# Performance work log

Measured on AMD Instinct MI355X. Metric: run time of the kernel, lower is better.

Reference implementation:

```python
import jax, jax.numpy as jnp
import numpy as np

B, C, H, W = 32, 3, 512, 512


def _make_rot(N):
    k = np.arange(N, dtype=np.float64)[None, :] * np.pi / (2 * N)
    return jnp.asarray(np.cos(k), jnp.float32), jnp.asarray(np.sin(k), jnp.float32)


def setup_inputs() -> dict:
    key = jax.random.key(0)
    X = jax.random.normal(key, (B, C, H, W), dtype=jnp.float32)
    W_r_weight, W_i_weight = _make_rot(W)
    W_r_height, W_i_height = _make_rot(H)
    return {
        "X": X,
        "W_r_weight": W_r_weight,
        "W_i_weight": W_i_weight,
        "W_r_height": W_r_height,
        "W_i_height": W_i_height,
    }


def _idct1(X, W_r, W_i):
    # 1D IDCT (DCT-III) along last axis via irfft, norm='ortho'.
    shp = X.shape
    N = shp[-1]
    Xv = X.reshape(-1, N) * 0.5
    # ortho scaling: col 0 -> *sqrt(N)*2, cols 1: -> *sqrt(N/2)*2 (after the /2)
    col_scale = np.full((N,), np.sqrt(N / 2) * 2, dtype=np.float32)
    col_scale[0] = np.sqrt(N) * 2
    Xv = Xv * jnp.asarray(col_scale)
    # V_t_i[:, 0] = 0; V_t_i[:, j] = -Xv[:, N-j] for j >= 1
    Vti = jnp.concatenate([jnp.zeros_like(Xv[:, :1]), -Xv[:, :0:-1]], axis=1)
    Vr = Xv * W_r - Vti * W_i
    Vi = Xv * W_i + Vti * W_r
    v = jnp.fft.irfft(jax.lax.complex(Vr, Vi), n=N, axis=1)  # [M, N] real
    # de-interleave: even outputs from front half, odd outputs from reversed tail
    x = jnp.zeros_like(v)
    x = x.at[:, ::2].set(v[:, : N - N // 2])
    x = x.at[:, 1::2].set(v[:, ::-1][:, : N // 2])
    return x.reshape(shp)


def reference(X, W_r_weight, W_i_weight, W_r_height, W_i_height):
    x = _idct1(X, W_r_weight, W_i_weight)          # IDCT over width
    x = jnp.swapaxes(x, -1, -2)
    x = _idct1(x, W_r_height, W_i_height)          # IDCT over height
    return jnp.swapaxes(x, -1, -2)
```

## Files before the change

### kernel.cpp

```cpp
#include <hip/hip_runtime.h>
#include <math.h>
#include <stdint.h>

#define N512 512

typedef __attribute__((ext_vector_type(8))) short short8;
typedef __attribute__((ext_vector_type(4))) float floatx4;

#define VMCNT0 asm volatile("s_waitcnt vmcnt(0)" ::: "memory")

__device__ __forceinline__ short f2bf(float f) {
    uint32_t u = __float_as_uint(f);
    uint32_t r = u + 0x7fffu + ((u >> 16) & 1u);
    return (short)(r >> 16);
}

__device__ __forceinline__ short f2bf_fast(float f) {
    return (short)((__float_as_uint(f) + 0x8000u) >> 16);
}

__device__ __forceinline__ void gload_lds16(const void* g, void* l) {
    __builtin_amdgcn_global_load_lds(
        (const __attribute__((address_space(1))) void*)g,
        (__attribute__((address_space(3))) void*)l,
        16, 0, 0);
}

__device__ __forceinline__ void decode_wave(int id, int& ms, int& ps, int& z) {
    const int g = (id >> 6) * 8 + (id & 7);
    ms = (id >> 3) & 7;
    ps = g & 7;
    z  = g >> 3;
}

__global__ __launch_bounds__(256) void build_idct_matrix_bf16(short* __restrict__ M) {
    int idx = blockIdx.x * 256 + threadIdx.x;
    int n = idx >> 9;
    int k = idx & 511;
    int j = (k * (2 * n + 1)) & (4 * N512 - 1);
    float theta = (float)j * (3.14159265358979323846f / (2.0f * (float)N512));
    float s = (k == 0) ? 0.044194173824159216f : 0.0625f;
    M[idx] = f2bf(s * cosf(theta));
}

__global__ __launch_bounds__(64) void gemm_s1(const short* __restrict__ A,
                                              const float* __restrict__ Xg,
                                              short* __restrict__ Tg) {
    __shared__ __align__(16) short ldsA[8 * 512];
    __shared__ __align__(16) short ldsB[8 * 512];

    const int l = threadIdx.x;
    const int q = (l >> 4) & 3;
    const int r = l & 15;

    int ms, ps, z;
    decode_wave(blockIdx.x, ms, ps, z);
    const int m0 = ms * 64;
    const int n0 = ps * 64;

    const float* Xs = Xg + ((long)z << 18);
    short* Tt = Tg + ((long)z << 18);

    const int rsub = l >> 3;
    const int glog = (l & 7) ^ rsub;

    const int brow = l >> 4;

    floatx4 acc[4][4] = {};
    float4 v[16];

    for (int kt = 0; kt < 8; ++kt) {
        const int k0 = kt * 64;
#pragma unroll
        for (int i = 0; i < 8; ++i)
            gload_lds16(A + (((long)(m0 + i * 8 + rsub)) << 9) + k0 + glog * 8,
                        ldsA + i * 512);
#pragma unroll
        for (int e = 0; e < 16; ++e) {
            const int rt = e * 4 + brow;
            v[e] = *(const float4*)(Xs + (((long)(n0 + rt)) << 9) + k0 + r * 4);
        }
        VMCNT0;
#pragma unroll
        for (int e = 0; e < 16; ++e) {
            const int rt = e * 4 + brow;
            short4 o;
            o.x = f2bf_fast(v[e].x);
            o.y = f2bf_fast(v[e].y);
            o.z = f2bf_fast(v[e].z);
            o.w = f2bf_fast(v[e].w);
            *(short4*)(ldsB + rt * 64 + (((r >> 1) ^ (rt & 7)) * 8) + (r & 1) * 4) = o;
        }
#pragma unroll
        for (int kk = 0; kk < 2; ++kk) {
            const int c = kk * 4 + q;
            const int goff = ((c ^ (r & 7)) * 8);
            short8 af[4], bfr[4];
#pragma unroll
            for (int i = 0; i < 4; ++i) {
                af[i]  = *(const short8*)(ldsA + (i * 16 + r) * 64 + goff);
                bfr[i] = *(const short8*)(ldsB + (i * 16 + r) * 64 + goff);
            }
#pragma unroll
            for (int i = 0; i < 4; ++i)
#pragma unroll
                for (int j = 0; j < 4; ++j)
                    acc[i][j] = __builtin_amdgcn_mfma_f32_16x16x32_bf16(
                        af[i], bfr[j], acc[i][j], 0, 0, 0);
        }
    }

#pragma unroll
    for (int i = 0; i < 4; ++i) {
        const int mrow = m0 + i * 16 + q * 4;
#pragma unroll
        for (int j = 0; j < 4; ++j) {
            const int ncol = n0 + j * 16 + r;
#pragma unroll
            for (int rg = 0; rg < 4; ++rg)
                Tt[(long)(mrow + rg) * N512 + ncol] = f2bf(acc[i][j][rg]);
        }
    }
}

__global__ __launch_bounds__(64) void gemm_s2(const short* __restrict__ A,
                                              const short* __restrict__ Bg,
                                              float* __restrict__ Cg) {
    __shared__ __align__(16) short ldsA[8 * 512];
    __shared__ __align__(16) short ldsB[8 * 512];

    const int l = threadIdx.x;
    const int q = (l >> 4) & 3;
    const int r = l & 15;

    int ms, ps, z;
    decode_wave(blockIdx.x, ms, ps, z);
    const int m0 = ms * 64;
    const int n0 = ps * 64;

    const short* Bs = Bg + ((long)z << 18);
    float* C = Cg + ((long)z << 18);

    const int rsub = l >> 3;
    const int glog = (l & 7) ^ rsub;

    floatx4 acc[4][4] = {};

    for (int kt = 0; kt < 8; ++kt) {
        const int k0 = kt * 64;
#pragma unroll
        for (int i = 0; i < 8; ++i) {
            gload_lds16(A + (((long)(m0 + i * 8 + rsub)) << 9) + k0 + glog * 8,
                        ldsA + i * 512);
            gload_lds16(Bs + (((long)(n0 + i * 8 + rsub)) << 9) + k0 + glog * 8,
                        ldsB + i * 512);
        }
        VMCNT0;
#pragma unroll
        for (int kk = 0; kk < 2; ++kk) {
            const int c = kk * 4 + q;
            const int goff = ((c ^ (r & 7)) * 8);
            short8 af[4], bfr[4];
#pragma unroll
            for (int i = 0; i < 4; ++i) {
                af[i]  = *(const short8*)(ldsA + (i * 16 + r) * 64 + goff);
                bfr[i] = *(const short8*)(ldsB + (i * 16 + r) * 64 + goff);
            }
#pragma unroll
            for (int i = 0; i < 4; ++i)
#pragma unroll
                for (int j = 0; j < 4; ++j)
                    acc[i][j] = __builtin_amdgcn_mfma_f32_16x16x32_bf16(
                        af[i], bfr[j], acc[i][j], 0, 0, 0);
        }
    }

#pragma unroll
    for (int i = 0; i < 4; ++i) {
        const int mrow = m0 + i * 16 + q * 4;
#pragma unroll
        for (int j = 0; j < 4; ++j) {
            const int ncol = n0 + j * 16 + r;
#pragma unroll
            for (int rg = 0; rg < 4; ++rg)
                C[(long)(mrow + rg) * N512 + ncol] = acc[i][j][rg];
        }
    }
}

extern "C" void kernel_launch(void* const* d_in, const int* in_sizes, int n_in,
                              void* d_out, int out_size, void* d_ws, size_t ws_size,
                              hipStream_t stream) {
    const float* X = (const float*)d_in[0];
    float* out = (float*)d_out;

    const long plane = (long)N512 * N512;
    const int slices = in_sizes[0] / (int)plane;

    short* Mb = (short*)d_ws;
    short* Tt = Mb + plane;

    long avail = (long)ws_size - plane * 2;
    int chunk = (int)(avail / (plane * 2));
    if (chunk > slices) chunk = slices;
    if (chunk < 1) chunk = 1;

    build_idct_matrix_bf16<<<dim3((int)(plane / 256)), dim3(256), 0, stream>>>(Mb);

    for (int s0 = 0; s0 < slices; s0 += chunk) {
        int c = (s0 + chunk <= slices) ? chunk : (slices - s0);
        gemm_s1<<<dim3(64 * c), dim3(64), 0, stream>>>(
            Mb, X + (long)s0 * plane, Tt);
        gemm_s2<<<dim3(64 * c), dim3(64), 0, stream>>>(
            Mb, Tt, out + (long)s0 * plane);
    }
}
```

Measured before the change: 259.1 us.

## Use 256x256 block tiles with 8 waves and double-buffered LDS pipelining

```diff
diff --git a/kernel.cpp b/kernel.cpp
--- a/kernel.cpp
+++ b/kernel.cpp
@@ -7,7 +7,9 @@
 typedef __attribute__((ext_vector_type(8))) short short8;
 typedef __attribute__((ext_vector_type(4))) float floatx4;
 
-#define VMCNT0 asm volatile("s_waitcnt vmcnt(0)" ::: "memory")
+#define VMCNT0  asm volatile("s_waitcnt vmcnt(0)" ::: "memory")
+#define LGKM0   asm volatile("s_waitcnt lgkmcnt(0)" ::: "memory")
+#define BARRIER __builtin_amdgcn_s_barrier()
 
 __device__ __forceinline__ short f2bf(float f) {
     uint32_t u = __float_as_uint(f);
@@ -24,13 +26,6 @@
         (const __attribute__((address_space(1))) void*)g,
         (__attribute__((address_space(3))) void*)l,
         16, 0, 0);
-}
-
-__device__ __forceinline__ void decode_wave(int id, int& ms, int& ps, int& z) {
-    const int g = (id >> 6) * 8 + (id & 7);
-    ms = (id >> 3) & 7;
-    ps = g & 7;
-    z  = g >> 3;
 }
 
 __global__ __launch_bounds__(256) void build_idct_matrix_bf16(short* __restrict__ M) {
@@ -43,20 +38,45 @@
     M[idx] = f2bf(s * cosf(theta));
 }
 
-__global__ __launch_bounds__(64) void gemm_s1(const short* __restrict__ A,
-                                              const float* __restrict__ Xg,
-                                              short* __restrict__ Tg) {
-    __shared__ __align__(16) short ldsA[8 * 512];
-    __shared__ __align__(16) short ldsB[8 * 512];
-
-    const int l = threadIdx.x;
+#define QUAD(MF)                                                                \
+    do {                                                                        \
+        short8 a00 = *(const short8*)(bufcA + (wm0 + (MF)*16 + r)*64 + gq0);    \
+        short8 a01 = *(const short8*)(bufcA + (wm0 + (MF)*16 + r)*64 + gq1);    \
+        short8 a10 = *(const short8*)(bufcA + (wm0 + (MF)*16 + 16 + r)*64 + gq0);\
+        short8 a11 = *(const short8*)(bufcA + (wm0 + (MF)*16 + 16 + r)*64 + gq1);\
+        __builtin_amdgcn_s_setprio(1);                                          \
+        _Pragma("unroll")                                                       \
+        for (int nf = 0; nf < 4; ++nf) {                                        \
+            acc[(MF)][nf]     = __builtin_amdgcn_mfma_f32_16x16x32_bf16(        \
+                a00, bfr[nf][0], acc[(MF)][nf], 0, 0, 0);                       \
+            acc[(MF)][nf]     = __builtin_amdgcn_mfma_f32_16x16x32_bf16(        \
+                a01, bfr[nf][1], acc[(MF)][nf], 0, 0, 0);                       \
+            acc[(MF) + 1][nf] = __builtin_amdgcn_mfma_f32_16x16x32_bf16(        \
+                a10, bfr[nf][0], acc[(MF) + 1][nf], 0, 0, 0);                   \
+            acc[(MF) + 1][nf] = __builtin_amdgcn_mfma_f32_16x16x32_bf16(        \
+                a11, bfr[nf][1], acc[(MF) + 1][nf], 0, 0, 0);                   \
+        }                                                                       \
+        __builtin_amdgcn_s_setprio(0);                                          \
+    } while (0)
+
+__global__ __launch_bounds__(512, 2) void gemm_s1(const short* __restrict__ A,
+                                                  const float* __restrict__ Xg,
+                                                  short* __restrict__ Tg) {
+    __shared__ __align__(16) short lds[2 * 32768];
+
+    const int t = threadIdx.x;
+    const int wv = t >> 6;
+    const int l = t & 63;
     const int q = (l >> 4) & 3;
     const int r = l & 15;
 
-    int ms, ps, z;
-    decode_wave(blockIdx.x, ms, ps, z);
-    const int m0 = ms * 64;
-    const int n0 = ps * 64;
+    const int id = blockIdx.x;
+    const int bn0 = (id & 1) * 256;
+    const int bm0 = ((id >> 1) & 1) * 256;
+    const int z = id >> 2;
+
+    const int wm0 = (wv >> 2) * 128;
+    const int wn0 = (wv & 3) * 64;
 
     const float* Xs = Xg + ((long)z << 18);
     short* Tt = Tg + ((long)z << 18);
@@ -64,79 +84,123 @@
     const int rsub = l >> 3;
     const int glog = (l & 7) ^ rsub;
 
-    const int brow = l >> 4;
-
-    floatx4 acc[4][4] = {};
-    float4 v[16];
+    const int trow = t >> 4;
+    const int tcol = t & 15;
+    const int bg = tcol >> 1;
+    const int bh = tcol & 1;
+
+    const int gq0 = ((q ^ (r & 7)) * 8);
+    const int gq1 = (((4 + q) ^ (r & 7)) * 8);
+
+    floatx4 acc[8][4] = {};
+    float4 v[8];
+
+#pragma unroll
+    for (int i = 0; i < 4; ++i) {
+        const int ch = wv * 4 + i;
+        gload_lds16(A + (((long)(bm0 + ch * 8 + rsub)) << 9) + glog * 8,
+                    lds + ch * 512);
+    }
+#pragma unroll
+    for (int p = 0; p < 8; ++p) {
+        const int rt = p * 32 + trow;
+        v[p] = *(const float4*)(Xs + (((long)(bn0 + rt)) << 9) + tcol * 4);
+    }
+    VMCNT0;
+#pragma unroll
+    for (int p = 0; p < 8; ++p) {
+        const int rt = p * 32 + trow;
+        short4 o;
+        o.x = f2bf_fast(v[p].x);
+        o.y = f2bf_fast(v[p].y);
+        o.z = f2bf_fast(v[p].z);
+        o.w = f2bf_fast(v[p].w);
+        *(short4*)(lds + 16384 + rt * 64 + ((bg ^ (rt & 7)) * 8) + bh * 4) = o;
+    }
+    LGKM0;
+    BARRIER;
 
     for (int kt = 0; kt < 8; ++kt) {
-        const int k0 = kt * 64;
-#pragma unroll
-        for (int i = 0; i < 8; ++i)
-            gload_lds16(A + (((long)(m0 + i * 8 + rsub)) << 9) + k0 + glog * 8,
-                        ldsA + i * 512);
-#pragma unroll
-        for (int e = 0; e < 16; ++e) {
-            const int rt = e * 4 + brow;
-            v[e] = *(const float4*)(Xs + (((long)(n0 + rt)) << 9) + k0 + r * 4);
-        }
-        VMCNT0;
-#pragma unroll
-        for (int e = 0; e < 16; ++e) {
-            const int rt = e * 4 + brow;
-            short4 o;
-            o.x = f2bf_fast(v[e].x);
-            o.y = f2bf_fast(v[e].y);
-            o.z = f2bf_fast(v[e].z);
-            o.w = f2bf_fast(v[e].w);
-            *(short4*)(ldsB + rt * 64 + (((r >> 1) ^ (rt & 7)) * 8) + (r & 1) * 4) = o;
-        }
-#pragma unroll
-        for (int kk = 0; kk < 2; ++kk) {
-            const int c = kk * 4 + q;
-            const int goff = ((c ^ (r & 7)) * 8);
-            short8 af[4], bfr[4];
+        short* bufcA = lds + (kt & 1) * 32768;
+        short* bufcB = bufcA + 16384;
+        short* bufnA = lds + ((kt + 1) & 1) * 32768;
+        short* bufnB = bufnA + 16384;
+
+        if (kt < 7) {
+            const int k0n = (kt + 1) * 64;
 #pragma unroll
             for (int i = 0; i < 4; ++i) {
-                af[i]  = *(const short8*)(ldsA + (i * 16 + r) * 64 + goff);
-                bfr[i] = *(const short8*)(ldsB + (i * 16 + r) * 64 + goff);
+                const int ch = wv * 4 + i;
+                gload_lds16(A + (((long)(bm0 + ch * 8 + rsub)) << 9) + k0n + glog * 8,
+                            bufnA + ch * 512);
             }
 #pragma unroll
-            for (int i = 0; i < 4; ++i)
-#pragma unroll
-                for (int j = 0; j < 4; ++j)
-                    acc[i][j] = __builtin_amdgcn_mfma_f32_16x16x32_bf16(
-                        af[i], bfr[j], acc[i][j], 0, 0, 0);
-        }
-    }
-
-#pragma unroll
-    for (int i = 0; i < 4; ++i) {
-        const int mrow = m0 + i * 16 + q * 4;
-#pragma unroll
-        for (int j = 0; j < 4; ++j) {
-            const int ncol = n0 + j * 16 + r;
+            for (int p = 0; p < 8; ++p) {
+                const int rt = p * 32 + trow;
+                v[p] = *(const float4*)(Xs + (((long)(bn0 + rt)) << 9) + k0n + tcol * 4);
+            }
+        }
+        short8 bfr[4][2];
+#pragma unroll
+        for (int nf = 0; nf < 4; ++nf) {
+            bfr[nf][0] = *(const short8*)(bufcB + (wn0 + nf * 16 + r) * 64 + gq0);
+            bfr[nf][1] = *(const short8*)(bufcB + (wn0 + nf * 16 + r) * 64 + gq1);
+        }
+        QUAD(0);
+        BARRIER;
+        QUAD(2);
+        BARRIER;
+        QUAD(4);
+        BARRIER;
+        QUAD(6);
+        if (kt < 7) {
+            VMCNT0;
+#pragma unroll
+            for (int p = 0; p < 8; ++p) {
+                const int rt = p * 32 + trow;
+                short4 o;
+                o.x = f2bf_fast(v[p].x);
+                o.y = f2bf_fast(v[p].y);
+                o.z = f2bf_fast(v[p].z);
+                o.w = f2bf_fast(v[p].w);
+                *(short4*)(bufnB + rt * 64 + ((bg ^ (rt & 7)) * 8) + bh * 4) = o;
+            }
+        }
+        LGKM0;
+        BARRIER;
+    }
+
+#pragma unroll
+    for (int mf = 0; mf < 8; ++mf) {
+        const int mrow = bm0 + wm0 + mf * 16 + q * 4;
+#pragma unroll
+        for (int nf = 0; nf < 4; ++nf) {
+            const int ncol = bn0 + wn0 + nf * 16 + r;
 #pragma unroll
             for (int rg = 0; rg < 4; ++rg)
-                Tt[(long)(mrow + rg) * N512 + ncol] = f2bf(acc[i][j][rg]);
-        }
-    }
-}
-
-__global__ __launch_bounds__(64) void gemm_s2(const short* __restrict__ A,
-                                              const short* __restrict__ Bg,
-                                              float* __restrict__ Cg) {
-    __shared__ __align__(16) short ldsA[8 * 512];
-    __shared__ __align__(16) short ldsB[8 * 512];
-
-    const int l = threadIdx.x;
+                Tt[(long)(mrow + rg) * N512 + ncol] = f2bf(acc[mf][nf][rg]);
+        }
+    }
+}
+
+__global__ __launch_bounds__(512, 2) void gemm_s2(const short* __restrict__ A,
+                                                  const short* __restrict__ Bg,
+                                                  float* __restrict__ Cg) {
+    __shared__ __align__(16) short lds[2 * 32768];
+
+    const int t = threadIdx.x;
+    const int wv = t >> 6;
+    const int l = t & 63;
     const int q = (l >> 4) & 3;
     const int r = l & 15;
 
-    int ms, ps, z;
-    decode_wave(blockIdx.x, ms, ps, z);
-    const int m0 = ms * 64;
-    const int n0 = ps * 64;
+    const int id = blockIdx.x;
+    const int bn0 = (id & 1) * 256;
+    const int bm0 = ((id >> 1) & 1) * 256;
+    const int z = id >> 2;
+
+    const int wm0 = (wv >> 2) * 128;
+    const int wn0 = (wv & 3) * 64;
 
     const short* Bs = Bg + ((long)z << 18);
     float* C = Cg + ((long)z << 18);
@@ -144,46 +208,65 @@
     const int rsub = l >> 3;
     const int glog = (l & 7) ^ rsub;
 
-    floatx4 acc[4][4] = {};
+    const int gq0 = ((q ^ (r & 7)) * 8);
+    const int gq1 = (((4 + q) ^ (r & 7)) * 8);
+
+    floatx4 acc[8][4] = {};
+
+#pragma unroll
+    for (int i = 0; i < 4; ++i) {
+        const int ch = wv * 4 + i;
+        gload_lds16(A + (((long)(bm0 + ch * 8 + rsub)) << 9) + glog * 8,
+                    lds + ch * 512);
+        gload_lds16(Bs + (((long)(bn0 + ch * 8 + rsub)) << 9) + glog * 8,
+                    lds + 16384 + ch * 512);
+    }
+    VMCNT0;
+    BARRIER;
 
     for (int kt = 0; kt < 8; ++kt) {
-        const int k0 = kt * 64;
-#pragma unroll
-        for (int i = 0; i < 8; ++i) {
-            gload_lds16(A + (((long)(m0 + i * 8 + rsub)) << 9) + k0 + glog * 8,
-                        ldsA + i * 512);
-            gload_lds16(Bs + (((long)(n0 + i * 8 + rsub)) << 9) + k0 + glog * 8,
-                        ldsB + i * 512);
-        }
-        VMCNT0;
-#pragma unroll
-        for (int kk = 0; kk < 2; ++kk) {
-            const int c = kk * 4 + q;
-            const int goff = ((c ^ (r & 7)) * 8);
-            short8 af[4], bfr[4];
+        short* bufcA = lds + (kt & 1) * 32768;
+        short* bufcB = bufcA + 16384;
+        short* bufnA = lds + ((kt + 1) & 1) * 32768;
+        short* bufnB = bufnA + 16384;
+
+        if (kt < 7) {
+            const int k0n = (kt + 1) * 64;
 #pragma unroll
             for (int i = 0; i < 4; ++i) {
-                af[i]  = *(const short8*)(ldsA + (i * 16 + r) * 64 + goff);
-                bfr[i] = *(const short8*)(ldsB + (i * 16 + r) * 64 + goff);
+                const int ch = wv * 4 + i;
+                gload_lds16(A + (((long)(bm0 + ch * 8 + rsub)) << 9) + k0n + glog * 8,
+                            bufnA + ch * 512);
+                gload_lds16(Bs + (((long)(bn0 + ch * 8 + rsub)) << 9) + k0n + glog * 8,
+                            bufnB + ch * 512);
             }
-#pragma unroll
-            for (int i = 0; i < 4; ++i)
-#pragma unroll
-                for (int j = 0; j < 4; ++j)
-                    acc[i][j] = __builtin_amdgcn_mfma_f32_16x16x32_bf16(
-                        af[i], bfr[j], acc[i][j], 0, 0, 0);
-        }
-    }
-
-#pragma unroll
-    for (int i = 0; i < 4; ++i) {
-        const int mrow = m0 + i * 16 + q * 4;
-#pragma unroll
-        for (int j = 0; j < 4; ++j) {
-            const int ncol = n0 + j * 16 + r;
+        }
+        short8 bfr[4][2];
+#pragma unroll
+        for (int nf = 0; nf < 4; ++nf) {
+            bfr[nf][0] = *(const short8*)(bufcB + (wn0 + nf * 16 + r) * 64 + gq0);
+            bfr[nf][1] = *(const short8*)(bufcB + (wn0 + nf * 16 + r) * 64 + gq1);
+        }
+        QUAD(0);
+        BARRIER;
+        QUAD(2);
+        BARRIER;
+        QUAD(4);
+        BARRIER;
+        QUAD(6);
+        if (kt < 7) VMCNT0;
+        BARRIER;
+    }
+
+#pragma unroll
+    for (int mf = 0; mf < 8; ++mf) {
+        const int mrow = bm0 + wm0 + mf * 16 + q * 4;
+#pragma unroll
+        for (int nf = 0; nf < 4; ++nf) {
+            const int ncol = bn0 + wn0 + nf * 16 + r;
 #pragma unroll
             for (int rg = 0; rg < 4; ++rg)
-                C[(long)(mrow + rg) * N512 + ncol] = acc[i][j][rg];
+                C[(long)(mrow + rg) * N512 + ncol] = acc[mf][nf][rg];
         }
     }
 }
@@ -209,9 +292,9 @@
 
     for (int s0 = 0; s0 < slices; s0 += chunk) {
         int c = (s0 + chunk <= slices) ? chunk : (slices - s0);
-        gemm_s1<<<dim3(64 * c), dim3(64), 0, stream>>>(
+        gemm_s1<<<dim3(4 * c), dim3(512), 0, stream>>>(
             Mb, X + (long)s0 * plane, Tt);
-        gemm_s2<<<dim3(64 * c), dim3(64), 0, stream>>>(
+        gemm_s2<<<dim3(4 * c), dim3(512), 0, stream>>>(
             Mb, Tt, out + (long)s0 * plane);
     }
 }
```

After: 246.3 us. 4.9% less time.
